# Performance work log

Hardware: AMD Instinct MI355X
Metric: run time of the kernel (lower is better)

Reference implementation:

```python
import jax, jax.numpy as jnp
import numpy as np

N, D, H, OUT, L = 4096, 127, 128, 3, 2
SIM_THRESH = 0.9
BN_EPS = 1e-5


def setup_inputs() -> dict:
    key = jax.random.key(0)
    ks = jax.random.split(key, 10)
    s = 1.0 / np.sqrt(H)
    x_now = jax.random.normal(ks[0], (N, D), dtype=jnp.float32)
    sat_type = jax.random.randint(ks[1], (N,), 0, 6, dtype=jnp.int64)
    # SAGEConv per layer: lin_l (neighbor aggr, with bias) and lin_r (root, no bias)
    Wl = jax.random.normal(ks[2], (L, H, H), dtype=jnp.float32) * s
    bl = jnp.zeros((L, H), dtype=jnp.float32)
    Wr = jax.random.normal(ks[3], (L, H, H), dtype=jnp.float32) * s
    gamma = jnp.ones((H,), dtype=jnp.float32)
    beta = jnp.zeros((H,), dtype=jnp.float32)
    Wo = jax.random.normal(ks[4], (OUT, H), dtype=jnp.float32) * s
    bo = jnp.zeros((OUT,), dtype=jnp.float32)
    return {"x_now": x_now, "sat_type": sat_type, "Wl": Wl, "bl": bl,
            "Wr": Wr, "gamma": gamma, "beta": beta, "Wo": Wo, "bo": bo}


def _forward(x_now, sat_type, Wl, bl, Wr, gamma, beta, Wo, bo):
    n = x_now.shape[0]
    # build_graph, h_prev=None branch: ppr = x_now[:, 0]
    x = jnp.concatenate([x_now[:, :1], x_now], axis=1)  # [N, H] with H = D+1
    # pairwise cosine similarity on first 4 features (F.normalize, eps=1e-12)
    f = x[:, :4]
    fn = f / jnp.maximum(jnp.linalg.norm(f, axis=1, keepdims=True), 1e-12)
    cos_sim = fn @ fn.T  # [N, N]
    same = sat_type[:, None] == sat_type[None, :]
    mask = (same | (cos_sim > SIM_THRESH)) & ~jnp.eye(n, dtype=bool)
    A = mask.astype(x.dtype)  # symmetric adjacency (dense form of edge list)
    deg = jnp.maximum(A.sum(axis=1, keepdims=True), 1.0)  # mean-aggr denom; isolated -> 0
    h = x
    for l in range(L):  # SAGEConv: lin_l(mean_j x_j) + lin_r(x_i), then ReLU
        m = (A @ h) / deg
        h = jax.nn.relu(m @ Wl[l].T + bl[l] + h @ Wr[l].T)
    # BatchNorm over nodes (training-mode batch stats, biased variance)
    mu = h.mean(axis=0)
    var = h.var(axis=0)
    h = (h - mu) / jnp.sqrt(var + BN_EPS) * gamma + beta
    out = h @ Wo.T + bo
    return h, out


def reference(x_now, sat_type, Wl, bl, Wr, gamma, beta, Wo, bo):
    return _forward(x_now, sat_type, Wl, bl, Wr, gamma, beta, Wo, bo)
```

## Files before the change

### kernel.cpp

```cpp
#include <hip/hip_runtime.h>
#include <math.h>

#define NN 4096
#define DD 127
#define HH 128
#define OUTD 3
#define NTYPES 6
#define SIM_THRESH 0.9f
#define BN_EPS 1e-5f
#define MROW 4
#define NREP 8
#define LMAXH 256

typedef unsigned short ushortT;
typedef __attribute__((ext_vector_type(8))) short short8;
typedef __attribute__((ext_vector_type(4))) float f32x4;
typedef __attribute__((ext_vector_type(2))) float f32x2;

static __device__ inline ushortT f2bf(float f) {
    unsigned u = __float_as_uint(f);
    unsigned r = (u + 0x7fffu + ((u >> 16) & 1u)) >> 16;
    return (ushortT)r;
}
static __device__ inline float bflo(unsigned w) { return __uint_as_float(w << 16); }
static __device__ inline float bfhi(unsigned w) { return __uint_as_float(w & 0xffff0000u); }

#define BFACC(vv)                                                         \
    {                                                                     \
        f32x2 t0 = {__uint_as_float((vv).x << 16),                        \
                    __uint_as_float((vv).x & 0xffff0000u)};               \
        f32x2 t1 = {__uint_as_float((vv).y << 16),                        \
                    __uint_as_float((vv).y & 0xffff0000u)};               \
        f32x2 t2 = {__uint_as_float((vv).z << 16),                        \
                    __uint_as_float((vv).z & 0xffff0000u)};               \
        f32x2 t3 = {__uint_as_float((vv).w << 16),                        \
                    __uint_as_float((vv).w & 0xffff0000u)};               \
        acc2[0] += t0; acc2[1] += t1; acc2[2] += t2; acc2[3] += t3;       \
    }

__global__ __launch_bounds__(256) void prep(
    const float* __restrict__ x_now, const int* __restrict__ sat,
    const float* __restrict__ Wl, const float* __restrict__ Wr,
    ushortT* __restrict__ Wbf, ushortT* __restrict__ xbf,
    float4* __restrict__ fn, int* __restrict__ cnt, float* __restrict__ S0rep)
{
    int t = threadIdx.x;
    if (blockIdx.x < 8) {
        int baseidx = blockIdx.x * 8192;
        #pragma unroll
        for (int it = 0; it < 32; ++it) {
            int idx = baseidx + it * 256 + t;
            float v = (idx < 32768) ? Wl[idx] : Wr[idx - 32768];
            Wbf[idx] = f2bf(v);
        }
        return;
    }

    int sb = blockIdx.x - 8;
    int base = sb * 16;
    int rep = sb & (NREP - 1);
    __shared__ int stypes[16];
    __shared__ float xs[16][HH];
    int myti = -1;
    if (t < 16) {
        int row = base + t;
        int ti = sat[row]; ti = min(max(ti, 0), NTYPES - 1);
        stypes[t] = ti; myti = ti;
        const float* rp = x_now + (size_t)row * DD;
        float f0 = rp[0], f2 = rp[1], f3 = rp[2];
        float nrm = fmaxf(sqrtf(2.f * f0 * f0 + f2 * f2 + f3 * f3), 1e-12f);
        float inv = 1.f / nrm;
        fn[row] = make_float4(f0 * inv, f0 * inv, f2 * inv, f3 * inv);
    }
    #pragma unroll
    for (int it = 0; it < 8; ++it) {
        int lin = it * 256 + t;
        int rl = lin >> 7, col = lin & 127;
        int row = base + rl;
        const float* rp = x_now + (size_t)row * DD;
        float v = (col == 0) ? rp[0] : rp[col - 1];
        xs[rl][col] = v;
        xbf[(size_t)row * HH + col] = f2bf(v);
    }
    __syncthreads();
    if (t < 64) {
        #pragma unroll
        for (int tt = 0; tt < NTYPES; ++tt) {
            unsigned long long m = __ballot(myti == tt);
            if (t == 0) {
                int c = __popcll(m);
                if (c) atomicAdd(&cnt[rep * NTYPES + tt], c);
            }
        }
    }
    if (t < 128) {
        float acc[NTYPES] = {0.f, 0.f, 0.f, 0.f, 0.f, 0.f};
        for (int r = 0; r < 16; ++r) {
            float v = xs[r][t];
            int tt = stypes[r];
            #pragma unroll
            for (int q = 0; q < NTYPES; ++q) acc[q] += (tt == q) ? v : 0.f;
        }
        #pragma unroll
        for (int q = 0; q < NTYPES; ++q)
            atomicAdd(&S0rep[(rep * NTYPES + q) * HH + t], acc[q]);
    }
}

__global__ __launch_bounds__(256) void build_mask(
    const float4* __restrict__ fn, const int* __restrict__ sat,
    const int* __restrict__ cnt, unsigned* __restrict__ mask,
    float* __restrict__ deg)
{
    int i0 = blockIdx.x * MROW;
    int t = threadIdx.x;
    int w = t & 127;
    int half = t >> 7;
    float4 fi[MROW];
    int ti[MROW];
    #pragma unroll
    for (int r = 0; r < MROW; ++r) {
        fi[r] = fn[i0 + r];
        int tt = sat[i0 + r];
        ti[r] = min(max(tt, 0), NTYPES - 1);
    }
    unsigned word[MROW] = {0, 0, 0, 0};
    int bbase = half * 16;
    for (int bb = 0; bb < 16; ++bb) {
        int b = bbase + bb;
        int j = b * 128 + w;
        float4 fj = fn[j];
        int tj = sat[j];
        #pragma unroll
        for (int r = 0; r < MROW; ++r) {
            float dot = fi[r].x * fj.x + fi[r].y * fj.y
                      + fi[r].z * fj.z + fi[r].w * fj.w;
            if (tj != ti[r] && dot > SIM_THRESH) word[r] |= (1u << b);
        }
    }
    __shared__ unsigned wpart[MROW][128];
    if (half == 1) {
        #pragma unroll
        for (int r = 0; r < MROW; ++r) wpart[r][w] = word[r];
    }
    __syncthreads();
    __shared__ int wt[2][MROW];
    if (half == 0) {
        int pcs[MROW];
        #pragma unroll
        for (int r = 0; r < MROW; ++r) {
            unsigned full = word[r] | wpart[r][w];
            mask[(size_t)(i0 + r) * 128 + w] = full;
            pcs[r] = __popc(full);
        }
        int lane = w & 63, wv2 = w >> 6;
        for (int s = 32; s; s >>= 1) {
            #pragma unroll
            for (int r = 0; r < MROW; ++r) pcs[r] += __shfl_down(pcs[r], s);
        }
        if (lane == 0) {
            #pragma unroll
            for (int r = 0; r < MROW; ++r) wt[wv2][r] = pcs[r];
        }
    }
    __syncthreads();
    if (t < MROW) {
        int r = t;
        int ctot = 0;
        #pragma unroll
        for (int rr = 0; rr < NREP; ++rr) ctot += cnt[rr * NTYPES + ti[r]];
        float d = (float)(ctot - 1 + wt[0][r] + wt[1][r]);
        deg[i0 + r] = fmaxf(d, 1.0f);
    }
}

__global__ __launch_bounds__(256, 6) void gather_kernel(
    const ushortT* __restrict__ hbf, const unsigned* __restrict__ mask,
    const float* __restrict__ deg, const float* __restrict__ S,
    const int* __restrict__ sat, ushortT* __restrict__ mbf)
{
    int t = threadIdx.x;
    int wv = t >> 6;
    int lane = t & 63;
    int r  = wv >> 1;
    int hf = wv & 1;
    int i0 = blockIdx.x * 2;
    int i = i0 + r;

    __shared__ ushortT list[4][LMAXH];
    __shared__ __align__(16) float part[4][HH];
    __shared__ int tarr[2];

    if (t < 2) {
        int tt = sat[i0 + t];
        tarr[t] = min(max(tt, 0), NTYPES - 1);
    }

    int widx = hf * 64 + lane;
    unsigned word = mask[(size_t)i * 128 + widx];
    int pc = __popc(word);
    int x = pc;
    for (int s = 1; s < 64; s <<= 1) {
        int v = __shfl_up(x, s);
        if (lane >= s) x += v;
    }
    int ncnt = __shfl(x, 63);
    int ofs = x - pc;
    unsigned ww = word;
    while (ww) {
        int b = __ffs(ww) - 1; ww &= ww - 1;
        list[wv][ofs++] = (ushortT)(b * 128 + widx);
    }

    int q = lane >> 4;
    int c = lane & 15;
    const uint4* __restrict__ hb4 = (const uint4*)hbf;
    f32x2 acc2[4] = {{0.f, 0.f}, {0.f, 0.f}, {0.f, 0.f}, {0.f, 0.f}};
    int g = 0;
    uint4 buf[6];
    if (g + 24 <= ncnt) {
        #pragma unroll
        for (int u = 0; u < 6; ++u)
            buf[u] = hb4[list[wv][g + u * 4 + q] * 16 + c];
    }
    for (; g + 48 <= ncnt; g += 24) {
        uint4 nbuf[6];
        #pragma unroll
        for (int u = 0; u < 6; ++u)
            nbuf[u] = hb4[list[wv][g + 24 + u * 4 + q] * 16 + c];
        #pragma unroll
        for (int u = 0; u < 6; ++u) { BFACC(buf[u]); }
        #pragma unroll
        for (int u = 0; u < 6; ++u) buf[u] = nbuf[u];
    }
    if (g + 24 <= ncnt) {
        #pragma unroll
        for (int u = 0; u < 6; ++u) { BFACC(buf[u]); }
        g += 24;
    }
    for (; g + 4 <= ncnt; g += 4) {
        int j0 = list[wv][g + q];
        uint4 v0 = hb4[j0 * 16 + c];
        BFACC(v0);
    }
    if (q < ncnt - g) {
        int j0 = list[wv][g + q];
        uint4 v0 = hb4[j0 * 16 + c];
        BFACC(v0);
    }
    #pragma unroll
    for (int d = 0; d < 4; ++d) {
        acc2[d].x += __shfl_down(acc2[d].x, 32);
        acc2[d].y += __shfl_down(acc2[d].y, 32);
        acc2[d].x += __shfl_down(acc2[d].x, 16);
        acc2[d].y += __shfl_down(acc2[d].y, 16);
    }
    if (lane < 16) {
        float4 p0 = {acc2[0].x, acc2[0].y, acc2[1].x, acc2[1].y};
        float4 p1 = {acc2[2].x, acc2[2].y, acc2[3].x, acc2[3].y};
        ((float4*)part[wv])[c * 2] = p0;
        ((float4*)part[wv])[c * 2 + 1] = p1;
    }
    __syncthreads();

    if (hf == 0 && lane < 32) {
        int cc = lane;
        float4 p0 = ((const float4*)part[wv])[cc];
        float4 p1 = ((const float4*)part[wv + 1])[cc];
        int ti = tarr[r];
        float rdeg = 1.f / deg[i];
        uint2 hw = ((const uint2*)(hbf + (size_t)i * HH))[cc];
        float4 hv = {bflo(hw.x), bfhi(hw.x), bflo(hw.y), bfhi(hw.y)};
        float4 Sv = {0.f, 0.f, 0.f, 0.f};
        #pragma unroll
        for (int rr = 0; rr < NREP; ++rr) {
            float4 sv = ((const float4*)S)[(rr * NTYPES + ti) * 32 + cc];
            Sv.x += sv.x; Sv.y += sv.y; Sv.z += sv.z; Sv.w += sv.w;
        }
        float4 m;
        m.x = (Sv.x - hv.x + p0.x + p1.x) * rdeg;
        m.y = (Sv.y - hv.y + p0.y + p1.y) * rdeg;
        m.z = (Sv.z - hv.z + p0.z + p1.z) * rdeg;
        m.w = (Sv.w - hv.w + p0.w + p1.w) * rdeg;
        ushort4 mb;
        mb.x = f2bf(m.x); mb.y = f2bf(m.y);
        mb.z = f2bf(m.z); mb.w = f2bf(m.w);
        ((ushort4*)(mbf + (size_t)i * HH))[cc] = mb;
    }
}

__global__ __launch_bounds__(512) void gemm_l1(
    const ushortT* __restrict__ mbf, const ushortT* __restrict__ hbf,
    const ushortT* __restrict__ Wlbf, const ushortT* __restrict__ Wrbf,
    const float* __restrict__ bl, const int* __restrict__ sat,
    ushortT* __restrict__ houtbf, float* __restrict__ acc0)
{
    int t = threadIdx.x;
    int wv = t >> 6, lane = t & 63;
    int p = lane & 15, q = lane >> 4;
    int i0 = blockIdx.x * 16;

    __shared__ float sh[16][129];
    __shared__ int stypes[16];
    if (t < 16) {
        int tt = sat[i0 + t];
        stypes[t] = min(max(tt, 0), NTYPES - 1);
    }

    const ushortT* arow_m = mbf + (size_t)(i0 + p) * HH + q * 8;
    const ushortT* arow_h = hbf + (size_t)(i0 + p) * HH + q * 8;
    short8 am[4], ah[4];
    #pragma unroll
    for (int s = 0; s < 4; ++s) {
        am[s] = *(const short8*)(arow_m + s * 32);
        ah[s] = *(const short8*)(arow_h + s * 32);
    }

    int n0 = wv * 16;
    const ushortT* brow_l = Wlbf + (size_t)(n0 + p) * HH + q * 8;
    const ushortT* brow_r = Wrbf + (size_t)(n0 + p) * HH + q * 8;
    f32x4 acc = {0.f, 0.f, 0.f, 0.f};
    #pragma unroll
    for (int s = 0; s < 4; ++s) {
        short8 b = *(const short8*)(brow_l + s * 32);
        acc = __builtin_amdgcn_mfma_f32_16x16x32_bf16(am[s], b, acc, 0, 0, 0);
    }
    #pragma unroll
    for (int s = 0; s < 4; ++s) {
        short8 b = *(const short8*)(brow_r + s * 32);
        acc = __builtin_amdgcn_mfma_f32_16x16x32_bf16(ah[s], b, acc, 0, 0, 0);
    }
    int o = n0 + p;
    float bv = bl[o];
    #pragma unroll
    for (int rg = 0; rg < 4; ++rg) {
        float v = fmaxf(acc[rg] + bv, 0.f);
        sh[q * 4 + rg][o] = v;
    }
    __syncthreads();

    #pragma unroll
    for (int e = 0; e < 4; ++e) {
        int lin = e * 512 + t;
        int rr = lin >> 7, cc = lin & 127;
        houtbf[(size_t)i0 * HH + lin] = f2bf(sh[rr][cc]);
    }
    int rep = blockIdx.x & (NREP - 1);
    if (t < HH) {
        float accq[NTYPES] = {0.f, 0.f, 0.f, 0.f, 0.f, 0.f};
        for (int r = 0; r < 16; ++r) {
            float v = sh[r][t];
            int tt = stypes[r];
            #pragma unroll
            for (int qq = 0; qq < NTYPES; ++qq)
                accq[qq] += (tt == qq) ? v : 0.f;
        }
        #pragma unroll
        for (int qq = 0; qq < NTYPES; ++qq)
            atomicAdd(&acc0[(rep * NTYPES + qq) * HH + t], accq[qq]);
    }
}

__global__ __launch_bounds__(512) void gemm_l2(
    const ushortT* __restrict__ mbf, const ushortT* __restrict__ hbf,
    const ushortT* __restrict__ Wlbf, const ushortT* __restrict__ Wrbf,
    const float* __restrict__ bl, float* __restrict__ hout,
    float* __restrict__ acc0, float* __restrict__ acc1)
{
    int t = threadIdx.x;
    int wv = t >> 6, lane = t & 63;
    int p = lane & 15, q = lane >> 4;
    int i0 = blockIdx.x * 16;

    __shared__ float sh[16][129];

    const ushortT* arow_m = mbf + (size_t)(i0 + p) * HH + q * 8;
    const ushortT* arow_h = hbf + (size_t)(i0 + p) * HH + q * 8;
    short8 am[4], ah[4];
    #pragma unroll
    for (int s = 0; s < 4; ++s) {
        am[s] = *(const short8*)(arow_m + s * 32);
        ah[s] = *(const short8*)(arow_h + s * 32);
    }

    int n0 = wv * 16;
    const ushortT* brow_l = Wlbf + (size_t)(n0 + p) * HH + q * 8;
    const ushortT* brow_r = Wrbf + (size_t)(n0 + p) * HH + q * 8;
    f32x4 acc = {0.f, 0.f, 0.f, 0.f};
    #pragma unroll
    for (int s = 0; s < 4; ++s) {
        short8 b = *(const short8*)(brow_l + s * 32);
        acc = __builtin_amdgcn_mfma_f32_16x16x32_bf16(am[s], b, acc, 0, 0, 0);
    }
    #pragma unroll
    for (int s = 0; s < 4; ++s) {
        short8 b = *(const short8*)(brow_r + s * 32);
        acc = __builtin_amdgcn_mfma_f32_16x16x32_bf16(ah[s], b, acc, 0, 0, 0);
    }
    int o = n0 + p;
    float bv = bl[o];
    #pragma unroll
    for (int rg = 0; rg < 4; ++rg) {
        float v = fmaxf(acc[rg] + bv, 0.f);
        sh[q * 4 + rg][o] = v;
    }
    __syncthreads();

    #pragma unroll
    for (int e = 0; e < 4; ++e) {
        int lin = e * 512 + t;
        int rr = lin >> 7, cc = lin & 127;
        hout[(size_t)i0 * HH + lin] = sh[rr][cc];
    }
    int rep = blockIdx.x & (NREP - 1);
    if (t < HH) {
        float s = 0.f, s2 = 0.f;
        for (int r = 0; r < 16; ++r) {
            float v = sh[r][t];
            s += v; s2 += v * v;
        }
        atomicAdd(&acc0[rep * HH + t], s);
        atomicAdd(&acc1[rep * HH + t], s2);
    }
}

__global__ __launch_bounds__(256) void finalize(
    const float* __restrict__ h, const float* __restrict__ musum8,
    const float* __restrict__ varsum8, const float* __restrict__ gamma,
    const float* __restrict__ beta, const float* __restrict__ Wo,
    const float* __restrict__ bo, float* __restrict__ out_h,
    float* __restrict__ out_o)
{
    int t = threadIdx.x;
    int wv = t >> 6;
    int lane = t & 63;
    int i = blockIdx.x * 4 + wv;

    float2 mus = {0.f, 0.f}, vas = {0.f, 0.f};
    #pragma unroll
    for (int r = 0; r < NREP; ++r) {
        float2 a = ((const float2*)(musum8 + r * HH))[lane];
        float2 b = ((const float2*)(varsum8 + r * HH))[lane];
        mus.x += a.x; mus.y += a.y;
        vas.x += b.x; vas.y += b.y;
    }
    float2 ga  = ((const float2*)gamma)[lane];
    float2 be  = ((const float2*)beta)[lane];
    float mu0 = mus.x * (1.f / NN), mu1 = mus.y * (1.f / NN);
    float v0 = vas.x * (1.f / NN) - mu0 * mu0;
    float v1 = vas.y * (1.f / NN) - mu1 * mu1;
    float sc0 = ga.x / sqrtf(v0 + BN_EPS), sc1 = ga.y / sqrtf(v1 + BN_EPS);
    float sh0 = be.x - mu0 * sc0, sh1 = be.y - mu1 * sc1;

    float2 hv = ((const float2*)(h + (size_t)i * HH))[lane];
    float2 hb;
    hb.x = hv.x * sc0 + sh0;
    hb.y = hv.y * sc1 + sh1;
    ((float2*)(out_h + (size_t)i * HH))[lane] = hb;

    float2 w0 = ((const float2*)Wo)[lane];
    float2 w1 = ((const float2*)(Wo + HH))[lane];
    float2 w2 = ((const float2*)(Wo + 2 * HH))[lane];
    float p0 = hb.x * w0.x + hb.y * w0.y;
    float p1 = hb.x * w1.x + hb.y * w1.y;
    float p2 = hb.x * w2.x + hb.y * w2.y;
    for (int s = 32; s; s >>= 1) {
        p0 += __shfl_down(p0, s);
        p1 += __shfl_down(p1, s);
        p2 += __shfl_down(p2, s);
    }
    if (lane == 0) {
        out_o[(size_t)i * OUTD + 0] = p0 + bo[0];
        out_o[(size_t)i * OUTD + 1] = p1 + bo[1];
        out_o[(size_t)i * OUTD + 2] = p2 + bo[2];
    }
}

extern "C" void kernel_launch(void* const* d_in, const int* in_sizes, int n_in,
                              void* d_out, int out_size, void* d_ws, size_t ws_size,
                              hipStream_t stream)
{
    (void)in_sizes; (void)n_in; (void)out_size; (void)ws_size;
    const float* x_now = (const float*)d_in[0];
    const int*   sat   = (const int*)d_in[1];
    const float* Wl    = (const float*)d_in[2];
    const float* bl    = (const float*)d_in[3];
    const float* Wr    = (const float*)d_in[4];
    const float* gamma = (const float*)d_in[5];
    const float* beta  = (const float*)d_in[6];
    const float* Wo    = (const float*)d_in[7];
    const float* bo    = (const float*)d_in[8];

    ushortT* Wbf  = (ushortT*)d_ws;
    ushortT* x0bf = Wbf + 65536;
    ushortT* h1bf = x0bf + (size_t)NN * HH;
    ushortT* mbf  = h1bf + (size_t)NN * HH;
    float* h2 = (float*)(mbf + (size_t)NN * HH);
    float4* fn = (float4*)(h2 + (size_t)NN * HH);
    unsigned* mask = (unsigned*)((float*)fn + 4 * NN);
    float* deg = (float*)(mask + (size_t)NN * 128);
    int*   cnt   = (int*)(deg + NN);
    float* S0rep = (float*)(cnt + 64);
    float* S1rep = S0rep + NREP * NTYPES * HH;
    float* mu8   = S1rep + NREP * NTYPES * HH;
    float* var8  = mu8 + NREP * HH;

    size_t zero_bytes = (64 + 2 * NREP * NTYPES * HH + 2 * NREP * HH)
                        * sizeof(float);
    hipMemsetAsync(cnt, 0, zero_bytes, stream);

    prep<<<264, 256, 0, stream>>>(x_now, sat, Wl, Wr, Wbf, x0bf, fn, cnt,
                                  S0rep);
    build_mask<<<NN / MROW, 256, 0, stream>>>(fn, sat, cnt, mask, deg);

    gather_kernel<<<NN / 2, 256, 0, stream>>>(x0bf, mask, deg, S0rep, sat,
                                              mbf);
    gemm_l1<<<NN / 16, 512, 0, stream>>>(mbf, x0bf, Wbf, Wbf + 32768, bl, sat,
                                         h1bf, S1rep);

    gather_kernel<<<NN / 2, 256, 0, stream>>>(h1bf, mask, deg, S1rep, sat,
                                              mbf);
    gemm_l2<<<NN / 16, 512, 0, stream>>>(mbf, h1bf, Wbf + 16384, Wbf + 49152,
                                         bl + HH, h2, mu8, var8);

    finalize<<<NN / 4, 256, 0, stream>>>(h2, mu8, var8, gamma, beta, Wo, bo,
                                         (float*)d_out, (float*)d_out + (size_t)NN * HH);
}
```

Baseline: 136.8 us.

## Replace sparse neighbor gather with dense MFMA aggregation over bitmask adjacency

```diff
diff --git a/kernel.cpp b/kernel.cpp
--- a/kernel.cpp
+++ b/kernel.cpp
@@ -10,39 +10,26 @@
 #define BN_EPS 1e-5f
 #define MROW 4
 #define NREP 8
-#define LMAXH 256
 
 typedef unsigned short ushortT;
 typedef __attribute__((ext_vector_type(8))) short short8;
 typedef __attribute__((ext_vector_type(4))) float f32x4;
-typedef __attribute__((ext_vector_type(2))) float f32x2;
 
 static __device__ inline ushortT f2bf(float f) {
     unsigned u = __float_as_uint(f);
     unsigned r = (u + 0x7fffu + ((u >> 16) & 1u)) >> 16;
     return (ushortT)r;
 }
-static __device__ inline float bflo(unsigned w) { return __uint_as_float(w << 16); }
-static __device__ inline float bfhi(unsigned w) { return __uint_as_float(w & 0xffff0000u); }
-
-#define BFACC(vv)                                                         \
-    {                                                                     \
-        f32x2 t0 = {__uint_as_float((vv).x << 16),                        \
-                    __uint_as_float((vv).x & 0xffff0000u)};               \
-        f32x2 t1 = {__uint_as_float((vv).y << 16),                        \
-                    __uint_as_float((vv).y & 0xffff0000u)};               \
-        f32x2 t2 = {__uint_as_float((vv).z << 16),                        \
-                    __uint_as_float((vv).z & 0xffff0000u)};               \
-        f32x2 t3 = {__uint_as_float((vv).w << 16),                        \
-                    __uint_as_float((vv).w & 0xffff0000u)};               \
-        acc2[0] += t0; acc2[1] += t1; acc2[2] += t2; acc2[3] += t3;       \
-    }
+static __device__ inline float bf2f(ushortT w) {
+    return __uint_as_float(((unsigned)w) << 16);
+}
 
 __global__ __launch_bounds__(256) void prep(
     const float* __restrict__ x_now, const int* __restrict__ sat,
     const float* __restrict__ Wl, const float* __restrict__ Wr,
     ushortT* __restrict__ Wbf, ushortT* __restrict__ xbf,
-    float4* __restrict__ fn, int* __restrict__ cnt, float* __restrict__ S0rep)
+    ushortT* __restrict__ xbfT, float4* __restrict__ fn,
+    int* __restrict__ cnt, float* __restrict__ S0rep)
 {
     int t = threadIdx.x;
     if (blockIdx.x < 8) {
@@ -83,6 +70,13 @@
         xbf[(size_t)row * HH + col] = f2bf(v);
     }
     __syncthreads();
+    {
+        int c = t >> 1, r0 = (t & 1) * 8;
+        short8 sv;
+        #pragma unroll
+        for (int k = 0; k < 8; ++k) sv[k] = (short)f2bf(xs[r0 + k][c]);
+        *(short8*)(xbfT + (size_t)c * NN + base + r0) = sv;
+    }
     if (t < 64) {
         #pragma unroll
         for (int tt = 0; tt < NTYPES; ++tt) {
@@ -109,7 +103,7 @@
 
 __global__ __launch_bounds__(256) void build_mask(
     const float4* __restrict__ fn, const int* __restrict__ sat,
-    const int* __restrict__ cnt, unsigned* __restrict__ mask,
+    const int* __restrict__ cnt, unsigned* __restrict__ maskT,
     float* __restrict__ deg)
 {
     int i0 = blockIdx.x * MROW;
@@ -146,21 +140,32 @@
     __syncthreads();
     __shared__ int wt[2][MROW];
     if (half == 0) {
+        int lane = w & 63, w01 = w >> 6;
+        unsigned full[MROW];
         int pcs[MROW];
         #pragma unroll
         for (int r = 0; r < MROW; ++r) {
-            unsigned full = word[r] | wpart[r][w];
-            mask[(size_t)(i0 + r) * 128 + w] = full;
-            pcs[r] = __popc(full);
-        }
-        int lane = w & 63, wv2 = w >> 6;
+            full[r] = word[r] | wpart[r][w];
+            pcs[r] = __popc(full[r]);
+        }
+        #pragma unroll
+        for (int r = 0; r < MROW; ++r) {
+            unsigned myw = 0;
+            for (int b = 0; b < 32; ++b) {
+                unsigned long long m = __ballot((full[r] >> b) & 1u);
+                if (lane == b)      myw = (unsigned)m;
+                if (lane == b + 32) myw = (unsigned)(m >> 32);
+            }
+            int W = (lane & 31) * 4 + w01 * 2 + (lane >> 5);
+            maskT[(size_t)(i0 + r) * 128 + W] = myw;
+        }
         for (int s = 32; s; s >>= 1) {
             #pragma unroll
             for (int r = 0; r < MROW; ++r) pcs[r] += __shfl_down(pcs[r], s);
         }
         if (lane == 0) {
             #pragma unroll
-            for (int r = 0; r < MROW; ++r) wt[wv2][r] = pcs[r];
+            for (int r = 0; r < MROW; ++r) wt[w01][r] = pcs[r];
         }
     }
     __syncthreads();
@@ -174,118 +179,87 @@
     }
 }
 
-__global__ __launch_bounds__(256, 6) void gather_kernel(
-    const ushortT* __restrict__ hbf, const unsigned* __restrict__ mask,
-    const float* __restrict__ deg, const float* __restrict__ S,
-    const int* __restrict__ sat, ushortT* __restrict__ mbf)
+__global__ __launch_bounds__(256) void agg(
+    const ushortT* __restrict__ HT, const ushortT* __restrict__ hbf,
+    const unsigned* __restrict__ maskT, const float* __restrict__ deg,
+    const float* __restrict__ S, const int* __restrict__ sat,
+    ushortT* __restrict__ mbf)
 {
     int t = threadIdx.x;
-    int wv = t >> 6;
-    int lane = t & 63;
-    int r  = wv >> 1;
-    int hf = wv & 1;
-    int i0 = blockIdx.x * 2;
-    int i = i0 + r;
-
-    __shared__ ushortT list[4][LMAXH];
-    __shared__ __align__(16) float part[4][HH];
-    __shared__ int tarr[2];
-
-    if (t < 2) {
+    int wv = t >> 6, lane = t & 63;
+    int p = lane & 15, q = lane >> 4;
+    int ib = blockIdx.x >> 2, cs = blockIdx.x & 3;
+    int i0 = ib * 16;
+    int c0 = cs * 32;
+
+    __shared__ unsigned smask[16][129];
+    __shared__ float red[4][2][64][4];
+    __shared__ float msum[16][33];
+    __shared__ int stypes[16];
+
+    #pragma unroll
+    for (int it = 0; it < 8; ++it) {
+        int lin = it * 256 + t;
+        int r = lin >> 7, w = lin & 127;
+        smask[r][w] = maskT[(size_t)(i0 + r) * 128 + w];
+    }
+    if (t < 16) {
         int tt = sat[i0 + t];
-        tarr[t] = min(max(tt, 0), NTYPES - 1);
-    }
-
-    int widx = hf * 64 + lane;
-    unsigned word = mask[(size_t)i * 128 + widx];
-    int pc = __popc(word);
-    int x = pc;
-    for (int s = 1; s < 64; s <<= 1) {
-        int v = __shfl_up(x, s);
-        if (lane >= s) x += v;
-    }
-    int ncnt = __shfl(x, 63);
-    int ofs = x - pc;
-    unsigned ww = word;
-    while (ww) {
-        int b = __ffs(ww) - 1; ww &= ww - 1;
-        list[wv][ofs++] = (ushortT)(b * 128 + widx);
-    }
-
-    int q = lane >> 4;
-    int c = lane & 15;
-    const uint4* __restrict__ hb4 = (const uint4*)hbf;
-    f32x2 acc2[4] = {{0.f, 0.f}, {0.f, 0.f}, {0.f, 0.f}, {0.f, 0.f}};
-    int g = 0;
-    uint4 buf[6];
-    if (g + 24 <= ncnt) {
-        #pragma unroll
-        for (int u = 0; u < 6; ++u)
-            buf[u] = hb4[list[wv][g + u * 4 + q] * 16 + c];
-    }
-    for (; g + 48 <= ncnt; g += 24) {
-        uint4 nbuf[6];
-        #pragma unroll
-        for (int u = 0; u < 6; ++u)
-            nbuf[u] = hb4[list[wv][g + 24 + u * 4 + q] * 16 + c];
-        #pragma unroll
-        for (int u = 0; u < 6; ++u) { BFACC(buf[u]); }
-        #pragma unroll
-        for (int u = 0; u < 6; ++u) buf[u] = nbuf[u];
-    }
-    if (g + 24 <= ncnt) {
-        #pragma unroll
-        for (int u = 0; u < 6; ++u) { BFACC(buf[u]); }
-        g += 24;
-    }
-    for (; g + 4 <= ncnt; g += 4) {
-        int j0 = list[wv][g + q];
-        uint4 v0 = hb4[j0 * 16 + c];
-        BFACC(v0);
-    }
-    if (q < ncnt - g) {
-        int j0 = list[wv][g + q];
-        uint4 v0 = hb4[j0 * 16 + c];
-        BFACC(v0);
-    }
-    #pragma unroll
-    for (int d = 0; d < 4; ++d) {
-        acc2[d].x += __shfl_down(acc2[d].x, 32);
-        acc2[d].y += __shfl_down(acc2[d].y, 32);
-        acc2[d].x += __shfl_down(acc2[d].x, 16);
-        acc2[d].y += __shfl_down(acc2[d].y, 16);
-    }
-    if (lane < 16) {
-        float4 p0 = {acc2[0].x, acc2[0].y, acc2[1].x, acc2[1].y};
-        float4 p1 = {acc2[2].x, acc2[2].y, acc2[3].x, acc2[3].y};
-        ((float4*)part[wv])[c * 2] = p0;
-        ((float4*)part[wv])[c * 2 + 1] = p1;
-    }
-    __syncthreads();
-
-    if (hf == 0 && lane < 32) {
-        int cc = lane;
-        float4 p0 = ((const float4*)part[wv])[cc];
-        float4 p1 = ((const float4*)part[wv + 1])[cc];
-        int ti = tarr[r];
+        stypes[t] = min(max(tt, 0), NTYPES - 1);
+    }
+    __syncthreads();
+
+    const ushortT* arow0 = HT + (size_t)(c0 + p) * NN + q * 8;
+    const ushortT* arow1 = HT + (size_t)(c0 + 16 + p) * NN + q * 8;
+    f32x4 acc0 = {0.f, 0.f, 0.f, 0.f};
+    f32x4 acc1 = {0.f, 0.f, 0.f, 0.f};
+    int sh0 = q * 8;
+    int sbase = wv * 32;
+    #pragma unroll 4
+    for (int s = 0; s < 32; ++s) {
+        int step = sbase + s;
+        int jbase = step * 32;
+        unsigned wm = smask[p][step] >> sh0;
+        short8 bv;
+        #pragma unroll
+        for (int jj = 0; jj < 8; ++jj)
+            bv[jj] = ((wm >> jj) & 1u) ? (short)0x3F80 : (short)0;
+        short8 a0 = *(const short8*)(arow0 + jbase);
+        short8 a1 = *(const short8*)(arow1 + jbase);
+        acc0 = __builtin_amdgcn_mfma_f32_16x16x32_bf16(a0, bv, acc0, 0, 0, 0);
+        acc1 = __builtin_amdgcn_mfma_f32_16x16x32_bf16(a1, bv, acc1, 0, 0, 0);
+    }
+    #pragma unroll
+    for (int rg = 0; rg < 4; ++rg) {
+        red[wv][0][lane][rg] = acc0[rg];
+        red[wv][1][lane][rg] = acc1[rg];
+    }
+    __syncthreads();
+    if (wv < 2) {
+        #pragma unroll
+        for (int rg = 0; rg < 4; ++rg) {
+            float tot = red[0][wv][lane][rg] + red[1][wv][lane][rg]
+                      + red[2][wv][lane][rg] + red[3][wv][lane][rg];
+            msum[p][wv * 16 + q * 4 + rg] = tot;
+        }
+    }
+    __syncthreads();
+
+    #pragma unroll
+    for (int e = 0; e < 2; ++e) {
+        int lin = e * 256 + t;
+        int r = lin >> 5, cl = lin & 31;
+        int c = c0 + cl;
+        int i = i0 + r;
+        int ti = stypes[r];
+        float Ssum = 0.f;
+        #pragma unroll
+        for (int rr = 0; rr < NREP; ++rr)
+            Ssum += S[(rr * NTYPES + ti) * HH + c];
+        float self = bf2f(hbf[(size_t)i * HH + c]);
         float rdeg = 1.f / deg[i];
-        uint2 hw = ((const uint2*)(hbf + (size_t)i * HH))[cc];
-        float4 hv = {bflo(hw.x), bfhi(hw.x), bflo(hw.y), bfhi(hw.y)};
-        float4 Sv = {0.f, 0.f, 0.f, 0.f};
-        #pragma unroll
-        for (int rr = 0; rr < NREP; ++rr) {
-            float4 sv = ((const float4*)S)[(rr * NTYPES + ti) * 32 + cc];
-            Sv.x += sv.x; Sv.y += sv.y; Sv.z += sv.z; Sv.w += sv.w;
-        }
-        float4 m;
-        m.x = (Sv.x - hv.x + p0.x + p1.x) * rdeg;
-        m.y = (Sv.y - hv.y + p0.y + p1.y) * rdeg;
-        m.z = (Sv.z - hv.z + p0.z + p1.z) * rdeg;
-        m.w = (Sv.w - hv.w + p0.w + p1.w) * rdeg;
-        ushort4 mb;
-        mb.x = f2bf(m.x); mb.y = f2bf(m.y);
-        mb.z = f2bf(m.z); mb.w = f2bf(m.w);
-        ((ushort4*)(mbf + (size_t)i * HH))[cc] = mb;
+        float m = (Ssum - self + msum[r][cl]) * rdeg;
+        mbf[(size_t)i * HH + c] = f2bf(m);
     }
 }
 
@@ -293,7 +267,8 @@
     const ushortT* __restrict__ mbf, const ushortT* __restrict__ hbf,
     const ushortT* __restrict__ Wlbf, const ushortT* __restrict__ Wrbf,
     const float* __restrict__ bl, const int* __restrict__ sat,
-    ushortT* __restrict__ houtbf, float* __restrict__ acc0)
+    ushortT* __restrict__ houtbf, ushortT* __restrict__ houtbfT,
+    float* __restrict__ acc0)
 {
     int t = threadIdx.x;
     int wv = t >> 6, lane = t & 63;
@@ -344,6 +319,15 @@
         int lin = e * 512 + t;
         int rr = lin >> 7, cc = lin & 127;
         houtbf[(size_t)i0 * HH + lin] = f2bf(sh[rr][cc]);
+    }
+    {
+        int c = t >> 2, r0 = (t & 3) * 4;
+        ushort4 uv;
+        uv.x = f2bf(sh[r0 + 0][c]);
+        uv.y = f2bf(sh[r0 + 1][c]);
+        uv.z = f2bf(sh[r0 + 2][c]);
+        uv.w = f2bf(sh[r0 + 3][c]);
+        *(ushort4*)(houtbfT + (size_t)c * NN + i0 + r0) = uv;
     }
     int rep = blockIdx.x & (NREP - 1);
     if (t < HH) {
@@ -491,14 +475,16 @@
     const float* Wo    = (const float*)d_in[7];
     const float* bo    = (const float*)d_in[8];
 
-    ushortT* Wbf  = (ushortT*)d_ws;
-    ushortT* x0bf = Wbf + 65536;
-    ushortT* h1bf = x0bf + (size_t)NN * HH;
-    ushortT* mbf  = h1bf + (size_t)NN * HH;
+    ushortT* Wbf   = (ushortT*)d_ws;
+    ushortT* x0bf  = Wbf + 65536;
+    ushortT* x0bfT = x0bf + (size_t)NN * HH;
+    ushortT* h1bf  = x0bfT + (size_t)NN * HH;
+    ushortT* h1bfT = h1bf + (size_t)NN * HH;
+    ushortT* mbf   = h1bfT + (size_t)NN * HH;
     float* h2 = (float*)(mbf + (size_t)NN * HH);
     float4* fn = (float4*)(h2 + (size_t)NN * HH);
-    unsigned* mask = (unsigned*)((float*)fn + 4 * NN);
-    float* deg = (float*)(mask + (size_t)NN * 128);
+    unsigned* maskT = (unsigned*)((float*)fn + 4 * NN);
+    float* deg = (float*)(maskT + (size_t)NN * 128);
     int*   cnt   = (int*)(deg + NN);
     float* S0rep = (float*)(cnt + 64);
     float* S1rep = S0rep + NREP * NTYPES * HH;
@@ -509,17 +495,17 @@
                         * sizeof(float);
     hipMemsetAsync(cnt, 0, zero_bytes, stream);
 
-    prep<<<264, 256, 0, stream>>>(x_now, sat, Wl, Wr, Wbf, x0bf, fn, cnt,
-                                  S0rep);
-    build_mask<<<NN / MROW, 256, 0, stream>>>(fn, sat, cnt, mask, deg);
-
-    gather_kernel<<<NN / 2, 256, 0, stream>>>(x0bf, mask, deg, S0rep, sat,
-                                              mbf);
+    prep<<<264, 256, 0, stream>>>(x_now, sat, Wl, Wr, Wbf, x0bf, x0bfT, fn,
+                                  cnt, S0rep);
+    build_mask<<<NN / MROW, 256, 0, stream>>>(fn, sat, cnt, maskT, deg);
+
+    agg<<<(NN / 16) * 4, 256, 0, stream>>>(x0bfT, x0bf, maskT, deg, S0rep,
+                                           sat, mbf);
     gemm_l1<<<NN / 16, 512, 0, stream>>>(mbf, x0bf, Wbf, Wbf + 32768, bl, sat,
-                                         h1bf, S1rep);
-
-    gather_kernel<<<NN / 2, 256, 0, stream>>>(h1bf, mask, deg, S1rep, sat,
-                                              mbf);
+                                         h1bf, h1bfT, S1rep);
+
+    agg<<<(NN / 16) * 4, 256, 0, stream>>>(h1bfT, h1bf, maskT, deg, S1rep,
+                                           sat, mbf);
     gemm_l2<<<NN / 16, 512, 0, stream>>>(mbf, h1bf, Wbf + 16384, Wbf + 49152,
                                          bl + HH, h2, mu8, var8);
 
```

After: 179.3 us. 1.31x slower.
